# Kernel tuning notes

Hardware: AMD Instinct MI355X
Metric: run time of the kernel (lower is better)

The kernel has to match this reference:

```python
import jax, jax.numpy as jnp
import numpy as np

N, M, K = 100000, 50000, 8   # num vertices, num hyperedges, fixed hyperedge size
DIN, DOUT = 128, 128

def setup_inputs() -> dict:
    key = jax.random.key(0)
    k1, k2, k3 = jax.random.split(key, 3)
    X = jax.random.normal(k1, (N, DIN), jnp.float32)
    vertex = jax.random.randint(k2, (M * K,), 0, N)          # member vertices, flattened
    edges = jnp.repeat(jnp.arange(M), K)                     # hyperedge id per entry (sorted)
    W = jax.random.normal(k3, (DIN, DOUT), jnp.float32) / np.sqrt(DIN)
    b = jnp.zeros((DOUT,), jnp.float32)
    return {"X": X, "vertex": vertex, "edges": edges, "W": W, "b": b}

def reference(X, vertex, edges, W, b):
    # theta: Linear(in, out) applied BEFORE graph construction (as in dhg.HyperGCNConv)
    Y = X @ W + b                              # [N, DOUT]
    verts = vertex.reshape(M, K)               # hyperedge membership (edges = repeat(arange(M), K))
    feats = Y[verts]                           # [M, K, DOUT] gather
    # pairwise squared distances within each hyperedge
    sq = jnp.sum(feats * feats, axis=-1)                      # [M, K]
    d2 = sq[:, :, None] + sq[:, None, :] - 2.0 * jnp.einsum('mkd,mld->mkl', feats, feats)
    flat = jnp.argmax(d2.reshape(M, K * K), axis=1)
    ui, vi = flat // K, flat % K                              # argmax-distance pair positions
    u = jnp.take_along_axis(verts, ui[:, None], 1)[:, 0]      # [M]
    v = jnp.take_along_axis(verts, vi[:, None], 1)[:, 0]      # [M]
    w = jnp.float32(1.0 / (2 * K - 3))                        # HyperGCN mediator weight
    pos = jnp.arange(K)
    med = ((pos[None, :] != ui[:, None]) & (pos[None, :] != vi[:, None])).astype(Y.dtype)  # [M,K]
    # graph edges: (u,v) + (u,m),(v,m) for each mediator m; masked entries get weight 0
    src = jnp.concatenate([u, jnp.repeat(u, K), jnp.repeat(v, K)])
    dst = jnp.concatenate([v, verts.reshape(-1), verts.reshape(-1)])
    wts = jnp.concatenate([jnp.full((M,), w, Y.dtype), (med * w).reshape(-1), (med * w).reshape(-1)])
    # GCN smoothing: D^{-1/2} (A + I) D^{-1/2} Y with symmetric A, duplicate edges summed
    deg = jnp.ones((N,), Y.dtype).at[src].add(wts).at[dst].add(wts)
    dinv = jax.lax.rsqrt(deg)
    Xs = Y * dinv[:, None]
    out = Xs                                                  # self-loop term
    out = out.at[dst].add(wts[:, None] * Xs[src])
    out = out.at[src].add(wts[:, None] * Xs[dst])
    out = out * dinv[:, None]
    return jax.nn.relu(out)                                   # is_last=False -> ReLU (dropout=0)
```

## Files before the change

### kernel.cpp

```cpp
#include <hip/hip_runtime.h>
#include <hip/hip_bf16.h>

#define NV 100000
#define ME 50000
#define NINC (ME * 8)
#define NBLK ((NV + 255) / 256)
#define NRBG ((NV + 127) / 128)
constexpr float WMED = 1.0f / 13.0f;

typedef __attribute__((ext_vector_type(8))) short bf16x8;
typedef __attribute__((ext_vector_type(4))) float f32x4;

static __device__ inline void cvt_split8(const float4& a, const float4& b,
                                         bf16x8& hi, bf16x8& lo) {
    const float v[8] = {a.x, a.y, a.z, a.w, b.x, b.y, b.z, b.w};
    #pragma unroll
    for (int j = 0; j < 8; ++j) {
        __hip_bfloat16 h = __float2bfloat16(v[j]);
        const float hf = __bfloat162float(h);
        __hip_bfloat16 l = __float2bfloat16(v[j] - hf);
        union { __hip_bfloat16 b; short s; } uh{h}, ul{l};
        hi[j] = uh.s;
        lo[j] = ul.s;
    }
}

__global__ __launch_bounds__(256) void k_wsplit(const float* __restrict__ W,
                                                short* __restrict__ Wg) {
    const int idx = blockIdx.x * 256 + threadIdx.x;
    const int k = idx >> 7;
    const int c = idx & 127;
    const float w = W[idx];
    __hip_bfloat16 h = __float2bfloat16(w);
    const float hf = __bfloat162float(h);
    __hip_bfloat16 l = __float2bfloat16(w - hf);
    const int cb = c >> 6, gp = (c >> 4) & 3, m = c & 15;
    const int s = k >> 5, qq = (k >> 3) & 3, j = k & 7;
    const int base = cb * 1024 + (s * 4 + gp) * 64 + qq * 16 + m;
    union { __hip_bfloat16 b; short s; } uh{h}, ul{l};
    Wg[(long)base * 8 + j] = uh.s;
    Wg[(long)(2048 + base) * 8 + j] = ul.s;
}

__global__ __launch_bounds__(256, 4) void k_gemm(const float* __restrict__ X,
                                                 const uint4* __restrict__ Wg,
                                                 const float* __restrict__ bias,
                                                 float* __restrict__ Y,
                                                 __hip_bfloat16* __restrict__ Ybf) {
    const int t = threadIdx.x;
    const int wv = t >> 6;
    const int L  = t & 63;
    const int m  = L & 15;
    const int q  = L >> 4;

    const int rb = blockIdx.x >> 1;
    const int cb = blockIdx.x & 1;

    const int row_base = rb * 128 + wv * 32;
    int r0 = row_base + m;      if (r0 > NV - 1) r0 = NV - 1;
    int r1 = row_base + 16 + m; if (r1 > NV - 1) r1 = NV - 1;
    const float* p0 = X + (long)r0 * 128 + q * 8;
    const float* p1 = X + (long)r1 * 128 + q * 8;

    const bf16x8* Whf = (const bf16x8*)Wg + cb * 1024;
    const bf16x8* Wlf = (const bf16x8*)Wg + 2048 + cb * 1024;

    f32x4 acc[2][4];
    #pragma unroll
    for (int tt = 0; tt < 2; ++tt)
        #pragma unroll
        for (int g = 0; g < 4; ++g)
            acc[tt][g] = (f32x4){0.f, 0.f, 0.f, 0.f};

    float4 Ac0 = *(const float4*)(p0);
    float4 Ac1 = *(const float4*)(p0 + 4);
    float4 Ac2 = *(const float4*)(p1);
    float4 Ac3 = *(const float4*)(p1 + 4);

    #pragma unroll
    for (int s = 0; s < 4; ++s) {
        float4 An0, An1, An2, An3;
        if (s < 3) {
            An0 = *(const float4*)(p0 + (s + 1) * 32);
            An1 = *(const float4*)(p0 + (s + 1) * 32 + 4);
            An2 = *(const float4*)(p1 + (s + 1) * 32);
            An3 = *(const float4*)(p1 + (s + 1) * 32 + 4);
        }
        bf16x8 ah0, al0, ah1, al1;
        cvt_split8(Ac0, Ac1, ah0, al0);
        cvt_split8(Ac2, Ac3, ah1, al1);
        #pragma unroll
        for (int g = 0; g < 4; ++g) {
            const bf16x8 bh = Whf[(s * 4 + g) * 64 + L];
            const bf16x8 bl = Wlf[(s * 4 + g) * 64 + L];
            acc[0][g] = __builtin_amdgcn_mfma_f32_16x16x32_bf16(ah0, bh, acc[0][g], 0, 0, 0);
            acc[0][g] = __builtin_amdgcn_mfma_f32_16x16x32_bf16(ah0, bl, acc[0][g], 0, 0, 0);
            acc[0][g] = __builtin_amdgcn_mfma_f32_16x16x32_bf16(al0, bh, acc[0][g], 0, 0, 0);
            acc[1][g] = __builtin_amdgcn_mfma_f32_16x16x32_bf16(ah1, bh, acc[1][g], 0, 0, 0);
            acc[1][g] = __builtin_amdgcn_mfma_f32_16x16x32_bf16(ah1, bl, acc[1][g], 0, 0, 0);
            acc[1][g] = __builtin_amdgcn_mfma_f32_16x16x32_bf16(al1, bh, acc[1][g], 0, 0, 0);
        }
        if (s < 3) { Ac0 = An0; Ac1 = An1; Ac2 = An2; Ac3 = An3; }
    }

    float bc[4];
    #pragma unroll
    for (int g = 0; g < 4; ++g) bc[g] = bias[cb * 64 + g * 16 + m];

    #pragma unroll
    for (int tt = 0; tt < 2; ++tt) {
        #pragma unroll
        for (int r = 0; r < 4; ++r) {
            const int row = row_base + tt * 16 + q * 4 + r;
            float vg[4], vn[4];
            #pragma unroll
            for (int g = 0; g < 4; ++g) {
                vg[g] = acc[tt][g][r] + bc[g];
                vn[g] = __shfl_xor(vg[g], 1);
            }
            if (row < NV) {
                #pragma unroll
                for (int g = 0; g < 4; ++g)
                    Y[(long)row * 128 + cb * 64 + g * 16 + m] = vg[g];
                if ((L & 1) == 0) {
                    #pragma unroll
                    for (int g = 0; g < 4; ++g) {
                        __hip_bfloat162 h2;
                        h2.x = __float2bfloat16(vg[g]);
                        h2.y = __float2bfloat16(vn[g]);
                        *(__hip_bfloat162*)(Ybf + (long)row * 128 + cb * 64 + g * 16 + m) = h2;
                    }
                }
            }
        }
    }
}

__global__ __launch_bounds__(256) void k_edge(const float* __restrict__ Y,
                                              const int* __restrict__ vertex,
                                              int* __restrict__ uvpos,
                                              int* __restrict__ cnt) {
    __shared__ float sF[4][8 * 132];
    const int wid = threadIdx.x >> 6;
    const int lane = threadIdx.x & 63;
    const int m = blockIdx.x * 4 + wid;
    float* F = sF[wid];

    int verts[8];
    #pragma unroll
    for (int p = 0; p < 8; ++p) verts[p] = vertex[m * 8 + p];

    if (lane < 8) atomicAdd(cnt + vertex[m * 8 + lane], 1);

    #pragma unroll
    for (int p = 0; p < 8; ++p) {
        const float2 v = *(const float2*)(Y + (long)verts[p] * 128 + lane * 2);
        *(float2*)(F + p * 132 + lane * 2) = v;
    }
    __syncthreads();

    const int k = lane >> 3, l = lane & 7;
    float acc = 0.0f;
    const float4* ra = (const float4*)(F + k * 132);
    const float4* rb = (const float4*)(F + l * 132);
    #pragma unroll
    for (int d4 = 0; d4 < 32; ++d4) {
        const float4 a = ra[d4], b = rb[d4];
        acc = fmaf(a.x, b.x, acc);
        acc = fmaf(a.y, b.y, acc);
        acc = fmaf(a.z, b.z, acc);
        acc = fmaf(a.w, b.w, acc);
    }
    const float sqk = __shfl(acc, k * 9);
    const float sql = __shfl(acc, l * 9);
    float v = sqk + sql - 2.0f * acc;
    int idx = lane;
    #pragma unroll
    for (int off = 32; off >= 1; off >>= 1) {
        const float ov = __shfl_xor(v, off);
        const int oi = __shfl_xor(idx, off);
        if (ov > v || (ov == v && oi < idx)) { v = ov; idx = oi; }
    }
    if (lane == 0) uvpos[m] = idx;
}

__global__ __launch_bounds__(256) void k_init(int* __restrict__ cnt,
                                              float* __restrict__ deg,
                                              int* __restrict__ rowptr) {
    const int i = blockIdx.x * 256 + threadIdx.x;
    if (i < NV) { cnt[i] = 0; deg[i] = 1.0f; }
    if (i == 0) rowptr[NV] = NINC;
}

__global__ __launch_bounds__(256) void k_scan1(const int* __restrict__ cnt,
                                               int* __restrict__ bsum) {
    __shared__ int s[256];
    const int t = threadIdx.x;
    const int i = blockIdx.x * 256 + t;
    s[t] = (i < NV) ? cnt[i] : 0;
    __syncthreads();
    #pragma unroll
    for (int off = 128; off >= 1; off >>= 1) {
        if (t < off) s[t] += s[t + off];
        __syncthreads();
    }
    if (t == 0) bsum[blockIdx.x] = s[0];
}

__global__ __launch_bounds__(64) void k_scan2(const int* __restrict__ bsum,
                                              int* __restrict__ boff) {
    const int lane = threadIdx.x;
    int running = 0;
    for (int c = 0; c * 64 < NBLK; ++c) {
        const int idx = c * 64 + lane;
        int v = (idx < NBLK) ? bsum[idx] : 0;
        int x = v;
        #pragma unroll
        for (int off = 1; off < 64; off <<= 1) {
            const int n = __shfl_up(x, off);
            if (lane >= off) x += n;
        }
        if (idx < NBLK) boff[idx] = running + x - v;
        running += __shfl(x, 63);
    }
}

__global__ __launch_bounds__(256) void k_scan3(const int* __restrict__ cnt,
                                               const int* __restrict__ boff,
                                               int* __restrict__ rowptr,
                                               int* __restrict__ fill) {
    __shared__ int s[256];
    const int t = threadIdx.x;
    const int i = blockIdx.x * 256 + t;
    const int v = (i < NV) ? cnt[i] : 0;
    s[t] = v;
    __syncthreads();
    #pragma unroll
    for (int off = 1; off < 256; off <<= 1) {
        const int add = (t >= off) ? s[t - off] : 0;
        __syncthreads();
        s[t] += add;
        __syncthreads();
    }
    if (i < NV) {
        const int excl = boff[blockIdx.x] + s[t] - v;
        rowptr[i] = excl;
        fill[i] = excl;
    }
}

__global__ __launch_bounds__(256) void k_fill(const int* __restrict__ vertex,
                                              const int* __restrict__ uvpos,
                                              int* __restrict__ fill,
                                              int* __restrict__ entries,
                                              float* __restrict__ deg) {
    const int j = blockIdx.x * 256 + threadIdx.x;
    if (j < NINC) {
        const int v = vertex[j];
        const int m = j >> 3, p = j & 7;
        const int idx = uvpos[m];
        const int role = (p == (idx >> 3) || p == (idx & 7)) ? 0 : 1;
        const int slot = atomicAdd(fill + v, 1);
        entries[slot] = (m << 1) | role;
        atomicAdd(deg + v, role ? (2.0f * WMED) : (7.0f * WMED));
    }
}

__global__ __launch_bounds__(256) void k_sp(const __hip_bfloat16* __restrict__ Ybf,
                                            const int* __restrict__ vertex,
                                            const int* __restrict__ uvpos,
                                            const float* __restrict__ deg,
                                            __hip_bfloat162* __restrict__ SP) {
    const int wid = threadIdx.x >> 6;
    const int lane = threadIdx.x & 63;
    const int m = blockIdx.x * 4 + wid;

    const int idx = uvpos[m];
    const int ui = idx >> 3, vi = idx & 7;

    float S0 = 0.f, S1 = 0.f, U0 = 0.f, U1 = 0.f, V0 = 0.f, V1 = 0.f;
    #pragma unroll
    for (int p = 0; p < 8; ++p) {
        const int vp = vertex[m * 8 + p];
        const float di = rsqrtf(deg[vp]);
        const __hip_bfloat162 y2 =
            ((const __hip_bfloat162*)(Ybf + (long)vp * 128))[lane];
        const float r0 = __bfloat162float(y2.x) * di;
        const float r1 = __bfloat162float(y2.y) * di;
        S0 += r0; S1 += r1;
        if (p == ui) { U0 = r0; U1 = r1; }
        if (p == vi) { V0 = r0; V1 = r1; }
    }
    __hip_bfloat162 s2, p2;
    s2.x = __float2bfloat16(WMED * S0);
    s2.y = __float2bfloat16(WMED * S1);
    p2.x = __float2bfloat16(WMED * (U0 + V0));
    p2.y = __float2bfloat16(WMED * (U1 + V1));
    SP[(long)(2 * m) * 64 + lane] = s2;
    SP[(long)(2 * m + 1) * 64 + lane] = p2;
}

__global__ __launch_bounds__(256) void k_gather(const float* __restrict__ Y,
                                                const float* __restrict__ deg,
                                                const int* __restrict__ rowptr,
                                                const int* __restrict__ entries,
                                                const __hip_bfloat162* __restrict__ SP,
                                                float* __restrict__ out) {
    const int wid = threadIdx.x >> 6;
    const int lane = threadIdx.x & 63;
    const int i = blockIdx.x * 4 + wid;

    const int start = rowptr[i], end = rowptr[i + 1];
    const int degc = end - start;
    const int tl = (lane < degc) ? entries[start + lane] : 0;

    const float din = rsqrtf(deg[i]);
    const float2 y = *(const float2*)(Y + (long)i * 128 + lane * 2);
    const float xs0 = y.x * din;
    const float xs1 = y.y * din;

    float a0 = 0.f, a1 = 0.f;
    float fnuv = 0.f;
    const int dmain = (degc < 64) ? degc : 64;

    for (int e = 0; e < dmain; e += 4) {
        const int j1 = (e + 1 < dmain) ? e + 1 : e;
        const int j2 = (e + 2 < dmain) ? e + 2 : e;
        const int j3 = (e + 3 < dmain) ? e + 3 : e;
        const float m1 = (e + 1 < dmain) ? 1.f : 0.f;
        const float m2 = (e + 2 < dmain) ? 1.f : 0.f;
        const float m3 = (e + 3 < dmain) ? 1.f : 0.f;
        const int t0 = __shfl(tl, e);
        const int t1 = __shfl(tl, j1);
        const int t2 = __shfl(tl, j2);
        const int t3 = __shfl(tl, j3);
        const __hip_bfloat162 T0 = SP[(long)t0 * 64 + lane];
        const __hip_bfloat162 T1 = SP[(long)t1 * 64 + lane];
        const __hip_bfloat162 T2 = SP[(long)t2 * 64 + lane];
        const __hip_bfloat162 T3 = SP[(long)t3 * 64 + lane];
        fnuv += (float)((t0 & 1) ^ 1) + m1 * (float)((t1 & 1) ^ 1)
              + m2 * (float)((t2 & 1) ^ 1) + m3 * (float)((t3 & 1) ^ 1);
        a0 += __bfloat162float(T0.x) + m1 * __bfloat162float(T1.x)
            + m2 * __bfloat162float(T2.x) + m3 * __bfloat162float(T3.x);
        a1 += __bfloat162float(T0.y) + m1 * __bfloat162float(T1.y)
            + m2 * __bfloat162float(T2.y) + m3 * __bfloat162float(T3.y);
    }
    for (int e2 = start + 64; e2 < end; ++e2) {
        const int t = entries[e2];
        const __hip_bfloat162 T = SP[(long)t * 64 + lane];
        fnuv += (float)((t & 1) ^ 1);
        a0 += __bfloat162float(T.x);
        a1 += __bfloat162float(T.y);
    }

    const float self = 1.0f - WMED * fnuv;
    a0 = fmaf(self, xs0, a0);
    a1 = fmaf(self, xs1, a1);
    float2 o;
    o.x = fmaxf(a0 * din, 0.0f);
    o.y = fmaxf(a1 * din, 0.0f);
    *(float2*)(out + (long)i * 128 + lane * 2) = o;
}

extern "C" void kernel_launch(void* const* d_in, const int* in_sizes, int n_in,
                              void* d_out, int out_size, void* d_ws, size_t ws_size,
                              hipStream_t stream) {
    const float* X      = (const float*)d_in[0];
    const int*   vertex = (const int*)d_in[1];
    const float* W      = (const float*)d_in[3];
    const float* bias   = (const float*)d_in[4];
    float* out = (float*)d_out;

    float* Y              = (float*)d_ws;
    __hip_bfloat16* Ybf   = (__hip_bfloat16*)(Y + (long)NV * 128);
    __hip_bfloat162* SP   = (__hip_bfloat162*)(Ybf + (long)NV * 128);
    float* deg            = (float*)((__hip_bfloat16*)SP + (long)2 * ME * 128);
    int*   uvpos          = (int*)(deg + NV);
    int*   cnt            = uvpos + ME;
    int*   rowptr         = cnt + NV;
    int*   fill           = rowptr + NV + 1;
    int*   bsum           = fill + NV;
    int*   boff           = bsum + NBLK;
    int*   entries        = boff + NBLK;
    char*  pW             = (char*)(entries + NINC);
    uint4* Wg             = (uint4*)(((uintptr_t)pW + 15) & ~(uintptr_t)15);

    k_wsplit<<<64, 256, 0, stream>>>(W, (short*)Wg);
    k_gemm <<<NRBG * 2, 256, 0, stream>>>(X, Wg, bias, Y, Ybf);
    k_init <<<NBLK, 256, 0, stream>>>(cnt, deg, rowptr);
    k_edge <<<ME / 4, 256, 0, stream>>>(Y, vertex, uvpos, cnt);
    k_scan1<<<NBLK, 256, 0, stream>>>(cnt, bsum);
    k_scan2<<<1, 64, 0, stream>>>(bsum, boff);
    k_scan3<<<NBLK, 256, 0, stream>>>(cnt, boff, rowptr, fill);
    k_fill <<<(NINC + 255) / 256, 256, 0, stream>>>(vertex, uvpos, fill, entries, deg);
    k_sp   <<<ME / 4, 256, 0, stream>>>(Ybf, vertex, uvpos, deg, SP);
    k_gather<<<NV / 4, 256, 0, stream>>>(Y, deg, rowptr, entries, SP, out);
}
```

Baseline: 271.9 us.

## Fuse weight split with init, drop scan2 pass, widen gather unroll to eight

Merges the weight bf16 hi/lo split kernel into the init kernel and removes the single-block scan2 by having each scan3 block sum the preceding block totals itself. This cuts two kernel launches and their inter-kernel gaps from the pipeline. The gather loop now handles eight neighbour entries per iteration instead of four, so more independent loads are in flight. In exchange, each scan3 block redundantly reads up to about 390 block sums, and the wider unroll uses more registers.

```diff
diff --git a/kernel.cpp b/kernel.cpp
--- a/kernel.cpp
+++ b/kernel.cpp
@@ -25,21 +25,28 @@
     }
 }
 
-__global__ __launch_bounds__(256) void k_wsplit(const float* __restrict__ W,
-                                                short* __restrict__ Wg) {
-    const int idx = blockIdx.x * 256 + threadIdx.x;
-    const int k = idx >> 7;
-    const int c = idx & 127;
-    const float w = W[idx];
-    __hip_bfloat16 h = __float2bfloat16(w);
-    const float hf = __bfloat162float(h);
-    __hip_bfloat16 l = __float2bfloat16(w - hf);
-    const int cb = c >> 6, gp = (c >> 4) & 3, m = c & 15;
-    const int s = k >> 5, qq = (k >> 3) & 3, j = k & 7;
-    const int base = cb * 1024 + (s * 4 + gp) * 64 + qq * 16 + m;
-    union { __hip_bfloat16 b; short s; } uh{h}, ul{l};
-    Wg[(long)base * 8 + j] = uh.s;
-    Wg[(long)(2048 + base) * 8 + j] = ul.s;
+__global__ __launch_bounds__(256) void k_winit(const float* __restrict__ W,
+                                               short* __restrict__ Wg,
+                                               int* __restrict__ cnt,
+                                               float* __restrict__ deg,
+                                               int* __restrict__ rowptr) {
+    const int i = blockIdx.x * 256 + threadIdx.x;
+    if (i < NV) { cnt[i] = 0; deg[i] = 1.0f; }
+    if (i == 0) rowptr[NV] = NINC;
+    if (i < 16384) {
+        const int k = i >> 7;
+        const int c = i & 127;
+        const float w = W[i];
+        __hip_bfloat16 h = __float2bfloat16(w);
+        const float hf = __bfloat162float(h);
+        __hip_bfloat16 l = __float2bfloat16(w - hf);
+        const int cb = c >> 6, gp = (c >> 4) & 3, m = c & 15;
+        const int s = k >> 5, qq = (k >> 3) & 3, j = k & 7;
+        const int base = cb * 1024 + (s * 4 + gp) * 64 + qq * 16 + m;
+        union { __hip_bfloat16 b; short s; } uh{h}, ul{l};
+        Wg[(long)base * 8 + j] = uh.s;
+        Wg[(long)(2048 + base) * 8 + j] = ul.s;
+    }
 }
 
 __global__ __launch_bounds__(256, 4) void k_gemm(const float* __restrict__ X,
@@ -184,14 +191,6 @@
     if (lane == 0) uvpos[m] = idx;
 }
 
-__global__ __launch_bounds__(256) void k_init(int* __restrict__ cnt,
-                                              float* __restrict__ deg,
-                                              int* __restrict__ rowptr) {
-    const int i = blockIdx.x * 256 + threadIdx.x;
-    if (i < NV) { cnt[i] = 0; deg[i] = 1.0f; }
-    if (i == 0) rowptr[NV] = NINC;
-}
-
 __global__ __launch_bounds__(256) void k_scan1(const int* __restrict__ cnt,
                                                int* __restrict__ bsum) {
     __shared__ int s[256];
@@ -207,33 +206,24 @@
     if (t == 0) bsum[blockIdx.x] = s[0];
 }
 
-__global__ __launch_bounds__(64) void k_scan2(const int* __restrict__ bsum,
-                                              int* __restrict__ boff) {
-    const int lane = threadIdx.x;
-    int running = 0;
-    for (int c = 0; c * 64 < NBLK; ++c) {
-        const int idx = c * 64 + lane;
-        int v = (idx < NBLK) ? bsum[idx] : 0;
-        int x = v;
-        #pragma unroll
-        for (int off = 1; off < 64; off <<= 1) {
-            const int n = __shfl_up(x, off);
-            if (lane >= off) x += n;
-        }
-        if (idx < NBLK) boff[idx] = running + x - v;
-        running += __shfl(x, 63);
-    }
-}
-
 __global__ __launch_bounds__(256) void k_scan3(const int* __restrict__ cnt,
-                                               const int* __restrict__ boff,
+                                               const int* __restrict__ bsum,
                                                int* __restrict__ rowptr,
                                                int* __restrict__ fill) {
     __shared__ int s[256];
+    __shared__ int base_s;
     const int t = threadIdx.x;
-    const int i = blockIdx.x * 256 + t;
+    const int b = blockIdx.x;
+    const int i = b * 256 + t;
     const int v = (i < NV) ? cnt[i] : 0;
     s[t] = v;
+    if (t < 64) {
+        int sum = 0;
+        for (int j = t; j < b; j += 64) sum += bsum[j];
+        #pragma unroll
+        for (int off = 32; off >= 1; off >>= 1) sum += __shfl_xor(sum, off);
+        if (t == 0) base_s = sum;
+    }
     __syncthreads();
     #pragma unroll
     for (int off = 1; off < 256; off <<= 1) {
@@ -243,7 +233,7 @@
         __syncthreads();
     }
     if (i < NV) {
-        const int excl = boff[blockIdx.x] + s[t] - v;
+        const int excl = base_s + s[t] - v;
         rowptr[i] = excl;
         fill[i] = excl;
     }
@@ -323,27 +313,49 @@
     float fnuv = 0.f;
     const int dmain = (degc < 64) ? degc : 64;
 
-    for (int e = 0; e < dmain; e += 4) {
+    for (int e = 0; e < dmain; e += 8) {
         const int j1 = (e + 1 < dmain) ? e + 1 : e;
         const int j2 = (e + 2 < dmain) ? e + 2 : e;
         const int j3 = (e + 3 < dmain) ? e + 3 : e;
+        const int j4 = (e + 4 < dmain) ? e + 4 : e;
+        const int j5 = (e + 5 < dmain) ? e + 5 : e;
+        const int j6 = (e + 6 < dmain) ? e + 6 : e;
+        const int j7 = (e + 7 < dmain) ? e + 7 : e;
         const float m1 = (e + 1 < dmain) ? 1.f : 0.f;
         const float m2 = (e + 2 < dmain) ? 1.f : 0.f;
         const float m3 = (e + 3 < dmain) ? 1.f : 0.f;
+        const float m4 = (e + 4 < dmain) ? 1.f : 0.f;
+        const float m5 = (e + 5 < dmain) ? 1.f : 0.f;
+        const float m6 = (e + 6 < dmain) ? 1.f : 0.f;
+        const float m7 = (e + 7 < dmain) ? 1.f : 0.f;
         const int t0 = __shfl(tl, e);
         const int t1 = __shfl(tl, j1);
         const int t2 = __shfl(tl, j2);
         const int t3 = __shfl(tl, j3);
+        const int t4 = __shfl(tl, j4);
+        const int t5 = __shfl(tl, j5);
+        const int t6 = __shfl(tl, j6);
+        const int t7 = __shfl(tl, j7);
         const __hip_bfloat162 T0 = SP[(long)t0 * 64 + lane];
         const __hip_bfloat162 T1 = SP[(long)t1 * 64 + lane];
         const __hip_bfloat162 T2 = SP[(long)t2 * 64 + lane];
         const __hip_bfloat162 T3 = SP[(long)t3 * 64 + lane];
+        const __hip_bfloat162 T4 = SP[(long)t4 * 64 + lane];
+        const __hip_bfloat162 T5 = SP[(long)t5 * 64 + lane];
+        const __hip_bfloat162 T6 = SP[(long)t6 * 64 + lane];
+        const __hip_bfloat162 T7 = SP[(long)t7 * 64 + lane];
         fnuv += (float)((t0 & 1) ^ 1) + m1 * (float)((t1 & 1) ^ 1)
-              + m2 * (float)((t2 & 1) ^ 1) + m3 * (float)((t3 & 1) ^ 1);
+              + m2 * (float)((t2 & 1) ^ 1) + m3 * (float)((t3 & 1) ^ 1)
+              + m4 * (float)((t4 & 1) ^ 1) + m5 * (float)((t5 & 1) ^ 1)
+              + m6 * (float)((t6 & 1) ^ 1) + m7 * (float)((t7 & 1) ^ 1);
         a0 += __bfloat162float(T0.x) + m1 * __bfloat162float(T1.x)
-            + m2 * __bfloat162float(T2.x) + m3 * __bfloat162float(T3.x);
+            + m2 * __bfloat162float(T2.x) + m3 * __bfloat162float(T3.x)
+            + m4 * __bfloat162float(T4.x) + m5 * __bfloat162float(T5.x)
+            + m6 * __bfloat162float(T6.x) + m7 * __bfloat162float(T7.x);
         a1 += __bfloat162float(T0.y) + m1 * __bfloat162float(T1.y)
-            + m2 * __bfloat162float(T2.y) + m3 * __bfloat162float(T3.y);
+            + m2 * __bfloat162float(T2.y) + m3 * __bfloat162float(T3.y)
+            + m4 * __bfloat162float(T4.y) + m5 * __bfloat162float(T5.y)
+            + m6 * __bfloat162float(T6.y) + m7 * __bfloat162float(T7.y);
     }
     for (int e2 = start + 64; e2 < end; ++e2) {
         const int t = entries[e2];
@@ -380,18 +392,15 @@
     int*   rowptr         = cnt + NV;
     int*   fill           = rowptr + NV + 1;
     int*   bsum           = fill + NV;
-    int*   boff           = bsum + NBLK;
-    int*   entries        = boff + NBLK;
+    int*   entries        = bsum + NBLK;
     char*  pW             = (char*)(entries + NINC);
     uint4* Wg             = (uint4*)(((uintptr_t)pW + 15) & ~(uintptr_t)15);
 
-    k_wsplit<<<64, 256, 0, stream>>>(W, (short*)Wg);
+    k_winit<<<NBLK, 256, 0, stream>>>(W, (short*)Wg, cnt, deg, rowptr);
     k_gemm <<<NRBG * 2, 256, 0, stream>>>(X, Wg, bias, Y, Ybf);
-    k_init <<<NBLK, 256, 0, stream>>>(cnt, deg, rowptr);
     k_edge <<<ME / 4, 256, 0, stream>>>(Y, vertex, uvpos, cnt);
     k_scan1<<<NBLK, 256, 0, stream>>>(cnt, bsum);
-    k_scan2<<<1, 64, 0, stream>>>(bsum, boff);
-    k_scan3<<<NBLK, 256, 0, stream>>>(cnt, boff, rowptr, fill);
+    k_scan3<<<NBLK, 256, 0, stream>>>(cnt, bsum, rowptr, fill);
     k_fill <<<(NINC + 255) / 256, 256, 0, stream>>>(vertex, uvpos, fill, entries, deg);
     k_sp   <<<ME / 4, 256, 0, stream>>>(Ybf, vertex, uvpos, deg, SP);
     k_gather<<<NV / 4, 256, 0, stream>>>(Y, deg, rowptr, entries, SP, out);
```

After: 266.8 us. Within noise of the previous version (-1.9%).
